# Kernel optimization log

Hardware: AMD Instinct MI355X
Metric: run time of the kernel (lower is better)

The kernel has to match this reference:

```python
import jax, jax.numpy as jnp
import numpy as np

EPS = 1e-12  # torch F.normalize eps


def setup_inputs() -> dict:
    key = jax.random.key(0)
    k1, k2, k3 = jax.random.split(key, 3)
    b, c, h, w = 4, 192, 128, 128
    num_heads = 8
    in1 = jax.random.normal(k1, (b, c, h, w), dtype=jnp.float32)
    in2 = jax.random.normal(k2, (b, c, h, w), dtype=jnp.float32)
    scale = jnp.ones((num_heads, 1, 1), dtype=jnp.float32)
    proj_w = jax.random.normal(k3, (c, c), dtype=jnp.float32) * (1.0 / np.sqrt(c))
    return {"in1": in1, "in2": in2, "scale": scale, "proj_w": proj_w, "num_heads": num_heads}


def reference(in1, in2, scale, proj_w, num_heads):
    b, c, h, w = in1.shape
    hd = c // num_heads
    hw = h * w
    # b (head c) h w -> b head c (h w)
    q = in1.reshape(b, num_heads, hd, hw)
    k = in2.reshape(b, num_heads, hd, hw)
    # L2-normalize along the (h w) axis, torch eps semantics
    q = q / jnp.maximum(jnp.linalg.norm(q, axis=-1, keepdims=True), EPS)
    k = k / jnp.maximum(jnp.linalg.norm(k, axis=-1, keepdims=True), EPS)
    # channel-wise attention: [b, head, c, c]
    attn = jnp.einsum('bhcn,bhdn->bhcd', q, k) * scale  # scale broadcasts [head,1,1]
    attn = jax.nn.softmax(attn, axis=-1)
    out = jnp.einsum('bhcd,bhdn->bhcn', attn, k)
    out = out.reshape(b, c, h, w)
    # 1x1 conv projection (no bias)
    out = jnp.einsum('oc,bchw->bohw', proj_w, out)
    return out
```

## Files before the change

kernel.cpp:

```cpp
#include <hip/hip_runtime.h>
#include <hip/hip_bf16.h>
#include <math.h>

#define BATCH 4
#define NHEAD 8
#define HD 24
#define CH 192
#define HW 16384
#define SPL 32
#define SROW 640

#define OFF_MO (32 * SPL * SROW)

#define LSTR 132

typedef __attribute__((ext_vector_type(8)))  short bf16x8;
typedef __attribute__((ext_vector_type(16))) float f32x16;

__device__ __forceinline__ unsigned short bf16rne(float x) {
    union { float f; unsigned u; } v; v.f = x;
    unsigned u = v.u;
    return (unsigned short)((u + 0x7FFFu + ((u >> 16) & 1u)) >> 16);
}

__device__ __forceinline__ unsigned pack2(float a, float b) {
    union { __hip_bfloat162 h; unsigned u; } c;
    c.h = __float22bfloat162_rn(float2{a, b});
    return c.u;
}

__global__ __launch_bounds__(256, 4) void kA(const float* __restrict__ q,
                                             const float* __restrict__ k,
                                             float* __restrict__ ws) {
    __shared__ unsigned int tile[2][HD * LSTR];

    const int bh   = blockIdx.x;
    const int ch   = blockIdx.y;
    const int t    = threadIdx.x;
    const int lane = t & 63;
    const int wave = t >> 6;
    const int m    = lane & 31;
    const int hi   = lane >> 5;
    const int rowc = (m < HD) ? m : 0;

    f32x16 aQK = {}, aQQ = {}, aKK = {};

    #pragma unroll
    for (int half = 0; half < 2; ++half) {
        const float* qb = q + (size_t)bh * HD * HW + ch * 512 + half * 256;
        const float* kb = k + (size_t)bh * HD * HW + ch * 512 + half * 256;

        #pragma unroll
        for (int j = 0; j < 6; ++j) {
            const int idx = j * 256 + t;
            const int row = idx >> 6;
            const int c64 = idx & 63;
            float4 qv = *(const float4*)(qb + (size_t)row * HW + c64 * 4);
            float4 kv = *(const float4*)(kb + (size_t)row * HW + c64 * 4);
            *(uint2*)&tile[0][row * LSTR + c64 * 2] =
                make_uint2(pack2(qv.x, qv.y), pack2(qv.z, qv.w));
            *(uint2*)&tile[1][row * LSTR + c64 * 2] =
                make_uint2(pack2(kv.x, kv.y), pack2(kv.z, kv.w));
        }
        __syncthreads();

        #pragma unroll
        for (int s = 0; s < 4; ++s) {
            const int off = (wave * 64 + s * 16) >> 1;
            bf16x8 aq = *(const bf16x8*)&tile[0][rowc * LSTR + off + hi * 4];
            bf16x8 bk = *(const bf16x8*)&tile[1][rowc * LSTR + off + hi * 4];
            aQK = __builtin_amdgcn_mfma_f32_32x32x16_bf16(aq, bk, aQK, 0, 0, 0);
            aQQ = __builtin_amdgcn_mfma_f32_32x32x16_bf16(aq, aq, aQQ, 0, 0, 0);
            aKK = __builtin_amdgcn_mfma_f32_32x32x16_bf16(bk, bk, aKK, 0, 0, 0);
        }
        __syncthreads();
    }

    float* red = (float*)tile;
    if (m < HD) {
        #pragma unroll
        for (int r = 0; r < 16; ++r) {
            const int i = (r & 3) + 8 * (r >> 2) + 4 * hi;
            if (i < HD) {
                red[wave * 624 + i * HD + m] = aQK[r];
                if (i == m) {
                    red[wave * 624 + 576 + i] = aQQ[r];
                    red[wave * 624 + 600 + i] = aKK[r];
                }
            }
        }
    }
    __syncthreads();

    float* Srow = ws + ((size_t)bh * SPL + ch) * SROW;
    for (int e = t; e < 624; e += 256)
        Srow[e] = red[e] + red[624 + e] + red[1248 + e] + red[1872 + e];
}

__global__ __launch_bounds__(1024) void kB(const float* __restrict__ scale,
                                           const float* __restrict__ w,
                                           float* __restrict__ ws,
                                           unsigned short* __restrict__ Mo) {
    const int bh = blockIdx.x;
    const int b  = bh >> 3;
    const int h  = bh & 7;
    const int t  = threadIdx.x;
    const int g  = t >> 8;
    const int u  = t & 255;

    __shared__ float part[4][624];
    __shared__ float SA[624];
    __shared__ float qinv[HD], kinv[HD];
    __shared__ float wl[CH * HD];

    const float* base = ws + (size_t)bh * SPL * SROW;

    float a0 = 0.f, a1 = 0.f, a2 = 0.f;
    for (int sp = g * 8; sp < g * 8 + 8; ++sp) {
        const float* r = base + (size_t)sp * SROW;
        a0 += r[u];
        a1 += r[u + 256];
        if (u < 112) a2 += r[u + 512];
    }
    part[g][u] = a0;
    part[g][u + 256] = a1;
    if (u < 112) part[g][u + 512] = a2;

    for (int idx = t; idx < CH * HD; idx += 1024) {
        int o = idx / HD, dd = idx % HD;
        wl[idx] = w[o * CH + h * HD + dd];
    }
    __syncthreads();

    if (t < 624) SA[t] = part[0][t] + part[1][t] + part[2][t] + part[3][t];
    __syncthreads();

    if (t < 2 * HD) {
        float inv = 1.0f / fmaxf(sqrtf(SA[576 + t]), 1e-12f);
        if (t < HD) qinv[t] = inv; else kinv[t - HD] = inv;
    }
    __syncthreads();

    const float sc = scale[h];
    if (t < 576) SA[t] = SA[t] * qinv[t / HD] * kinv[t % HD] * sc;
    __syncthreads();

    if (t < HD) {
        float m = -1e30f;
        for (int j = 0; j < HD; ++j) m = fmaxf(m, SA[t * HD + j]);
        float sum = 0.f;
        for (int j = 0; j < HD; ++j) {
            float v = expf(SA[t * HD + j] - m);
            SA[t * HD + j] = v;
            sum += v;
        }
        float r = 1.0f / sum;
        for (int j = 0; j < HD; ++j) SA[t * HD + j] *= r;
    }
    __syncthreads();

    for (int idx = t; idx < CH * HD; idx += 1024) {
        int o = idx / HD, j = idx % HD;
        float v = 0.f;
        #pragma unroll
        for (int i = 0; i < HD; ++i) v = fmaf(wl[o * HD + i], SA[i * HD + j], v);
        Mo[(size_t)b * CH * CH + (size_t)o * CH + h * HD + j] = bf16rne(v * kinv[j]);
    }
}

#define KCN 64
#define BSTR3 100

__global__ __launch_bounds__(256, 4) void kC(const float* __restrict__ k,
                                             const unsigned short* __restrict__ Mo,
                                             float* __restrict__ out) {
    __shared__ unsigned int Bt[KCN * BSTR3];

    const int t    = threadIdx.x;
    const int lane = t & 63;
    const int wave = t >> 6;
    const int n31  = lane & 31;
    const int hi   = lane >> 5;
    const int nt   = wave & 1;
    const int otb  = (wave >> 1) * 3;

    const int nb = blockIdx.x * KCN;
    const int b  = blockIdx.y;

    const float* kb = k + (size_t)b * CH * HW;
    const unsigned short* Mob = Mo + (size_t)b * CH * CH;

    const int np4 = t & 15;
    const int cg4 = t >> 4;

    #pragma unroll
    for (int s = 0; s < 3; ++s) {
        float4 v[4];
        #pragma unroll
        for (int cc = 0; cc < 4; ++cc)
            v[cc] = *(const float4*)(kb + (size_t)(s * 64 + cg4 * 4 + cc) * HW + nb + np4 * 4);
        #pragma unroll
        for (int r = 0; r < 4; ++r) {
            float x0 = (&v[0].x)[r], x1 = (&v[1].x)[r];
            float x2 = (&v[2].x)[r], x3 = (&v[3].x)[r];
            *(uint2*)&Bt[(np4 * 4 + r) * BSTR3 + s * 32 + cg4 * 2] =
                make_uint2(pack2(x0, x1), pack2(x2, x3));
        }
    }
    __syncthreads();

    f32x16 acc[3] = {};
    #pragma unroll
    for (int kc = 0; kc < 12; ++kc) {
        bf16x8 Bf = *(const bf16x8*)&Bt[(nt * 32 + n31) * BSTR3 + kc * 8 + hi * 4];
        #pragma unroll
        for (int oi = 0; oi < 3; ++oi) {
            const unsigned short* ap =
                Mob + (size_t)((otb + oi) * 32 + n31) * CH + kc * 16 + hi * 8;
            bf16x8 Af = *(const bf16x8*)ap;
            acc[oi] = __builtin_amdgcn_mfma_f32_32x32x16_bf16(Af, Bf, acc[oi], 0, 0, 0);
        }
    }

    float* op = out + (size_t)b * CH * HW;
    const int n = nb + nt * 32 + n31;
    #pragma unroll
    for (int oi = 0; oi < 3; ++oi)
        #pragma unroll
        for (int r = 0; r < 16; ++r) {
            int o = (otb + oi) * 32 + (r & 3) + 8 * (r >> 2) + 4 * hi;
            op[(size_t)o * HW + n] = acc[oi][r];
        }
}

extern "C" void kernel_launch(void* const* d_in, const int* in_sizes, int n_in,
                              void* d_out, int out_size, void* d_ws, size_t ws_size,
                              hipStream_t stream) {
    const float* in1   = (const float*)d_in[0];
    const float* in2   = (const float*)d_in[1];
    const float* scale = (const float*)d_in[2];
    const float* projw = (const float*)d_in[3];
    float* ws  = (float*)d_ws;
    float* out = (float*)d_out;
    unsigned short* Mo = (unsigned short*)(ws + OFF_MO);

    kA<<<dim3(32, SPL), 256, 0, stream>>>(in1, in2, ws);
    kB<<<32, 1024, 0, stream>>>(scale, projw, ws, Mo);
    kC<<<dim3(HW / KCN, BATCH), 256, 0, stream>>>(in2, Mo, out);
}
```

Baseline: 175.4 us.

## Fuse reduction/softmax kernel into kA via last-block atomic counter

Removes the separate kB launch. Each kA block increments a per-(batch,head) atomic counter after writing its partial Gram rows. The last block to arrive then reduces the 32 splits, normalizes, runs the softmax and computes the projected bf16 matrix Mo in reused shared memory. This saves a kernel boundary, but it adds a memset of the counters and serializes the tail work onto one 256-thread block per head instead of a 1024-thread block.

```diff
diff --git a/kernel.cpp b/kernel.cpp
--- a/kernel.cpp
+++ b/kernel.cpp
@@ -10,7 +10,8 @@
 #define SPL 32
 #define SROW 640
 
-#define OFF_MO (32 * SPL * SROW)
+#define OFF_MO  (32 * SPL * SROW)
+#define OFF_CNT (OFF_MO + (BATCH * CH * CH) / 2)
 
 #define LSTR 132
 
@@ -31,8 +32,13 @@
 
 __global__ __launch_bounds__(256, 4) void kA(const float* __restrict__ q,
                                              const float* __restrict__ k,
-                                             float* __restrict__ ws) {
+                                             const float* __restrict__ scale,
+                                             const float* __restrict__ w,
+                                             float* __restrict__ ws,
+                                             unsigned short* __restrict__ Mo,
+                                             unsigned int* __restrict__ cnt) {
     __shared__ unsigned int tile[2][HD * LSTR];
+    __shared__ int lastFlag;
 
     const int bh   = blockIdx.x;
     const int ch   = blockIdx.y;
@@ -95,76 +101,71 @@
     float* Srow = ws + ((size_t)bh * SPL + ch) * SROW;
     for (int e = t; e < 624; e += 256)
         Srow[e] = red[e] + red[624 + e] + red[1248 + e] + red[1872 + e];
-}
-
-__global__ __launch_bounds__(1024) void kB(const float* __restrict__ scale,
-                                           const float* __restrict__ w,
-                                           float* __restrict__ ws,
-                                           unsigned short* __restrict__ Mo) {
-    const int bh = blockIdx.x;
-    const int b  = bh >> 3;
-    const int h  = bh & 7;
-    const int t  = threadIdx.x;
-    const int g  = t >> 8;
-    const int u  = t & 255;
-
-    __shared__ float part[4][624];
-    __shared__ float SA[624];
-    __shared__ float qinv[HD], kinv[HD];
-    __shared__ float wl[CH * HD];
-
+
+    __syncthreads();
+    if (t == 0) {
+        unsigned int old = __hip_atomic_fetch_add(&cnt[bh], 1u,
+                                                  __ATOMIC_ACQ_REL,
+                                                  __HIP_MEMORY_SCOPE_AGENT);
+        lastFlag = (old == SPL - 1);
+    }
+    __syncthreads();
+    if (!lastFlag) return;
+
+    float* sf = (float*)tile;
+    const int b = bh >> 3;
+    const int h = bh & 7;
     const float* base = ws + (size_t)bh * SPL * SROW;
 
-    float a0 = 0.f, a1 = 0.f, a2 = 0.f;
-    for (int sp = g * 8; sp < g * 8 + 8; ++sp) {
-        const float* r = base + (size_t)sp * SROW;
-        a0 += r[u];
-        a1 += r[u + 256];
-        if (u < 112) a2 += r[u + 512];
-    }
-    part[g][u] = a0;
-    part[g][u + 256] = a1;
-    if (u < 112) part[g][u + 512] = a2;
-
-    for (int idx = t; idx < CH * HD; idx += 1024) {
-        int o = idx / HD, dd = idx % HD;
-        wl[idx] = w[o * CH + h * HD + dd];
-    }
-    __syncthreads();
-
-    if (t < 624) SA[t] = part[0][t] + part[1][t] + part[2][t] + part[3][t];
+    for (int idx = t; idx < CH * HD; idx += 256) {
+        int o = idx / HD, dd = idx - o * HD;
+        sf[672 + idx] = w[o * CH + h * HD + dd];
+    }
+    for (int e = t; e < 624; e += 256) {
+        float s0 = 0.f, s1 = 0.f, s2 = 0.f, s3 = 0.f;
+        #pragma unroll
+        for (int sp = 0; sp < SPL; sp += 4) {
+            s0 += base[(size_t)(sp + 0) * SROW + e];
+            s1 += base[(size_t)(sp + 1) * SROW + e];
+            s2 += base[(size_t)(sp + 2) * SROW + e];
+            s3 += base[(size_t)(sp + 3) * SROW + e];
+        }
+        sf[e] = (s0 + s1) + (s2 + s3);
+    }
     __syncthreads();
 
     if (t < 2 * HD) {
-        float inv = 1.0f / fmaxf(sqrtf(SA[576 + t]), 1e-12f);
-        if (t < HD) qinv[t] = inv; else kinv[t - HD] = inv;
+        float inv = 1.0f / fmaxf(sqrtf(sf[576 + t]), 1e-12f);
+        sf[624 + t] = inv;
     }
     __syncthreads();
 
     const float sc = scale[h];
-    if (t < 576) SA[t] = SA[t] * qinv[t / HD] * kinv[t % HD] * sc;
+    for (int e = t; e < 576; e += 256)
+        sf[e] = sf[e] * sf[624 + e / HD] * sf[648 + e % HD] * sc;
     __syncthreads();
 
     if (t < HD) {
-        float m = -1e30f;
-        for (int j = 0; j < HD; ++j) m = fmaxf(m, SA[t * HD + j]);
+        float mx = -1e30f;
+        for (int j = 0; j < HD; ++j) mx = fmaxf(mx, sf[t * HD + j]);
         float sum = 0.f;
         for (int j = 0; j < HD; ++j) {
-            float v = expf(SA[t * HD + j] - m);
-            SA[t * HD + j] = v;
+            float v = expf(sf[t * HD + j] - mx);
+            sf[t * HD + j] = v;
             sum += v;
         }
         float r = 1.0f / sum;
-        for (int j = 0; j < HD; ++j) SA[t * HD + j] *= r;
-    }
-    __syncthreads();
-
-    for (int idx = t; idx < CH * HD; idx += 1024) {
-        int o = idx / HD, j = idx % HD;
+        for (int j = 0; j < HD; ++j) sf[t * HD + j] *= r;
+    }
+    __syncthreads();
+
+    for (int idx = t; idx < CH * HD; idx += 256) {
+        int o = idx / HD, j = idx - o * HD;
         float v = 0.f;
         #pragma unroll
-        for (int i = 0; i < HD; ++i) v = fmaf(wl[o * HD + i], SA[i * HD + j], v);
-        Mo[(size_t)b * CH * CH + (size_t)o * CH + h * HD + j] = bf16rne(v * kinv[j]);
+        for (int i = 0; i < HD; ++i)
+            v = fmaf(sf[672 + o * HD + i], sf[i * HD + j], v);
+        Mo[(size_t)b * CH * CH + (size_t)o * CH + h * HD + j] = bf16rne(v * sf[648 + j]);
     }
 }
 
@@ -243,8 +244,9 @@
     float* ws  = (float*)d_ws;
     float* out = (float*)d_out;
     unsigned short* Mo = (unsigned short*)(ws + OFF_MO);
-
-    kA<<<dim3(32, SPL), 256, 0, stream>>>(in1, in2, ws);
-    kB<<<32, 1024, 0, stream>>>(scale, projw, ws, Mo);
+    unsigned int* cnt  = (unsigned int*)(ws + OFF_CNT);
+
+    hipMemsetAsync((void*)cnt, 0, 32 * sizeof(unsigned int), stream);
+    kA<<<dim3(32, SPL), 256, 0, stream>>>(in1, in2, scale, projw, ws, Mo, cnt);
     kC<<<dim3(HW / KCN, BATCH), 256, 0, stream>>>(in2, Mo, out);
 }
```

After: 222.1 us. 1.27x slower.
